# Optimization experiments

Measured on AMD Instinct MI355X. Metric: run time of the kernel, lower is better.

## Reference

```python
import jax, jax.numpy as jnp
import numpy as np

ORDER = 3  # polynomial filter order


def _sketch_conv(x, A, W, b, coeffs):
    # z = A @ (x W + b); out = sum_d coeffs[d-1] * z**d  (Horner-free power accumulation)
    z = A @ (x @ W + b)            # [N, out_c]
    p = z
    acc = coeffs[0] * z
    for d in range(1, ORDER):      # small fixed loop over polynomial order
        p = p * z
        acc = acc + coeffs[d] * p
    return acc


def setup_inputs() -> dict:
    key = jax.random.key(0)
    ks = jax.random.split(key, 12)
    N, C_IN, C_H, C_OUT = 8192, 128, 64, 40
    nf_mats = jax.random.normal(ks[0], (N, C_IN), dtype=jnp.float32)
    # scale by 1/sqrt(N) so polynomial powers stay O(1)
    conv_mats = jax.random.normal(ks[1], (N, N), dtype=jnp.float32) / np.float32(np.sqrt(N))
    def lin(k, fi, fo):
        kw, kb = jax.random.split(k)
        W = jax.random.normal(kw, (fi, fo), dtype=jnp.float32) / np.float32(np.sqrt(fi))
        b = jax.random.normal(kb, (fo,), dtype=jnp.float32) * np.float32(0.01)
        return W, b
    W1, b1 = lin(ks[2], C_IN, C_H)
    W2, b2 = lin(ks[3], C_H, C_H)
    W3, b3 = lin(ks[4], C_H, C_OUT)
    base = jnp.array([1.0, 0.0, 0.0], dtype=jnp.float32)
    c1 = base + jax.random.normal(ks[5], (ORDER,), dtype=jnp.float32) * 0.05
    c2 = base + jax.random.normal(ks[6], (ORDER,), dtype=jnp.float32) * 0.05
    c3 = base + jax.random.normal(ks[7], (ORDER,), dtype=jnp.float32) * 0.05
    return {"nf_mats": nf_mats, "conv_mats": conv_mats,
            "W1": W1, "b1": b1, "c1": c1,
            "W2": W2, "b2": b2, "c2": c2,
            "W3": W3, "b3": b3, "c3": c3}


def reference(nf_mats, conv_mats, W1, b1, c1, W2, b2, c2, W3, b3, c3):
    # SketchGCN eval-mode forward: batchnorm=False, dropout inactive.
    x = _sketch_conv(nf_mats, conv_mats, W1, b1, c1)      # first layer
    x = x + _sketch_conv(x, conv_mats, W2, b2, c2)        # residual middle layer
    return _sketch_conv(x, conv_mats, W3, b3, c3)         # output layer
```

## Files before the change

kernel.cpp:

```cpp
#include <hip/hip_runtime.h>
#include <stdint.h>

typedef __bf16 bf16x8 __attribute__((ext_vector_type(8)));
typedef float f32x4 __attribute__((ext_vector_type(4)));

using gvoid = const __attribute__((address_space(1))) void;
using lvoid = __attribute__((address_space(3))) void;

__device__ __forceinline__ unsigned short f2bf(float f) {
    union { float f; unsigned u; } x; x.f = f;
    unsigned u = x.u;
    u += 0x7FFFu + ((u >> 16) & 1u);
    return (unsigned short)(u >> 16);
}

__global__ void convert_bf16(const float* __restrict__ in,
                             unsigned short* __restrict__ out, int nv4) {
    int idx = blockIdx.x * blockDim.x + threadIdx.x;
    int stride = gridDim.x * blockDim.x;
    const float4* in4 = (const float4*)in;
    ushort4* out4 = (ushort4*)out;
    for (int i = idx; i < nv4; i += stride) {
        float4 v = in4[i];
        ushort4 o;
        o.x = f2bf(v.x); o.y = f2bf(v.y); o.z = f2bf(v.z); o.w = f2bf(v.w);
        out4[i] = o;
    }
}

template <int CIN>
__global__ __launch_bounds__(256) void small_gemm(const float* __restrict__ X,
                                                  const float* __restrict__ W,
                                                  const float* __restrict__ b,
                                                  int cout,
                                                  unsigned short* __restrict__ Yt) {
    __shared__ float Xs[64 * (CIN + 1)];
    __shared__ float Ws[CIN * 64];
    __shared__ float bs[64];
    const int t = threadIdx.x;
    const int i0 = blockIdx.x * 64;

    for (int e = t; e < 64 * CIN; e += 256) {
        int r = e / CIN, c = e % CIN;
        Xs[r * (CIN + 1) + c] = X[(size_t)(i0 + r) * CIN + c];
    }
    for (int e = t; e < CIN * 64; e += 256) {
        int k = e >> 6, j = e & 63;
        Ws[e] = (j < cout) ? W[k * cout + j] : 0.0f;
    }
    if (t < 64) bs[t] = (t < cout) ? b[t] : 0.0f;
    __syncthreads();

    const int i = t & 63;
    const int jg = t >> 6;
    float acc[16];
#pragma unroll
    for (int jj = 0; jj < 16; ++jj) acc[jj] = 0.0f;

    for (int k = 0; k < CIN; ++k) {
        float xv = Xs[i * (CIN + 1) + k];
        const float4* wr = (const float4*)&Ws[k * 64 + jg * 16];
#pragma unroll
        for (int q = 0; q < 4; ++q) {
            float4 w = wr[q];
            acc[q * 4 + 0] += xv * w.x;
            acc[q * 4 + 1] += xv * w.y;
            acc[q * 4 + 2] += xv * w.z;
            acc[q * 4 + 3] += xv * w.w;
        }
    }
#pragma unroll
    for (int jj = 0; jj < 16; ++jj) {
        int j = jg * 16 + jj;
        Yt[(size_t)j * 8192 + i0 + i] = f2bf(acc[jj] + bs[j]);
    }
}

__global__ __launch_bounds__(256) void big_gemm(const unsigned short* __restrict__ Ab,
                                                const unsigned short* __restrict__ Yt,
                                                float* __restrict__ P) {
    __shared__ unsigned short As[2][128 * 64];
    __shared__ unsigned short Bs[2][64 * 64];
    const int t = threadIdx.x;
    const int lane = t & 63, wid = t >> 6;
    const int lane15 = lane & 15, lane4 = lane >> 4;
    const int wm = wid >> 1, wn = wid & 1;
    const int row0 = blockIdx.x * 128;
    const int kbase = blockIdx.y * 2048;

    f32x4 acc[4][2];
    const f32x4 z4 = {0.f, 0.f, 0.f, 0.f};
#pragma unroll
    for (int m = 0; m < 4; ++m)
#pragma unroll
        for (int n = 0; n < 2; ++n) acc[m][n] = z4;

    auto stage = [&](int nb, int kt) {
#pragma unroll
        for (int ii = 0; ii < 4; ++ii) {
            int p = ii * 256 + wid * 64 + lane;
            int r = p >> 3;
            int c = (p & 7) ^ (r & 7);
            const unsigned short* gp = Ab + (size_t)(row0 + r) * 8192 + (kt + c * 8);
            unsigned short* lp = &As[nb][(ii * 256 + wid * 64) * 8];
            __builtin_amdgcn_global_load_lds((gvoid*)gp, (lvoid*)lp, 16, 0, 0);
        }
#pragma unroll
        for (int ii = 0; ii < 2; ++ii) {
            int q = ii * 256 + wid * 64 + lane;
            int n = q >> 3;
            int c = (q & 7) ^ (n & 7);
            const unsigned short* gp = Yt + (size_t)n * 8192 + (kt + c * 8);
            unsigned short* lp = &Bs[nb][(ii * 256 + wid * 64) * 8];
            __builtin_amdgcn_global_load_lds((gvoid*)gp, (lvoid*)lp, 16, 0, 0);
        }
    };

    stage(0, kbase);
    __syncthreads();
    int buf = 0;
    for (int tt = 0; tt < 32; ++tt) {
        if (tt + 1 < 32) stage(buf ^ 1, kbase + (tt + 1) * 64);
#pragma unroll
        for (int ks = 0; ks < 2; ++ks) {
            bf16x8 af[4], bfr[2];
#pragma unroll
            for (int m = 0; m < 4; ++m) {
                int r = wm * 64 + m * 16 + lane15;
                int c = ks * 4 + lane4;
                af[m] = *(const bf16x8*)&As[buf][((r << 3) | (c ^ (r & 7))) << 3];
            }
#pragma unroll
            for (int n = 0; n < 2; ++n) {
                int rn = wn * 32 + n * 16 + lane15;
                int c = ks * 4 + lane4;
                bfr[n] = *(const bf16x8*)&Bs[buf][((rn << 3) | (c ^ (rn & 7))) << 3];
            }
#pragma unroll
            for (int m = 0; m < 4; ++m)
#pragma unroll
                for (int n = 0; n < 2; ++n)
                    acc[m][n] = __builtin_amdgcn_mfma_f32_16x16x32_bf16(
                        af[m], bfr[n], acc[m][n], 0, 0, 0);
        }
        __syncthreads();
        buf ^= 1;
    }

    float* Po = P + (size_t)blockIdx.y * (8192 * 64);
#pragma unroll
    for (int m = 0; m < 4; ++m) {
        int r = row0 + wm * 64 + m * 16 + lane4 * 4;
#pragma unroll
        for (int n = 0; n < 2; ++n) {
            int cc = wn * 32 + n * 16 + lane15;
#pragma unroll
            for (int q = 0; q < 4; ++q)
                Po[(size_t)(r + q) * 64 + cc] = acc[m][n][q];
        }
    }
}

template <int MODE>
__global__ void reduce_poly(const float* __restrict__ P, const float* __restrict__ cf,
                            const float* __restrict__ xres, float* __restrict__ out) {
    int t = blockIdx.x * 256 + threadIdx.x;
    const int NT = 8192 * 64;
    float z = P[t] + P[t + NT] + P[t + 2 * NT] + P[t + 3 * NT];
    float c0 = cf[0], c1 = cf[1], c2 = cf[2];
    float v = z * (c0 + z * (c1 + z * c2));
    if (MODE == 1) v += xres[t];
    if (MODE == 2) {
        int i = t >> 6, j = t & 63;
        if (j < 40) out[(size_t)i * 40 + j] = v;
    } else {
        out[t] = v;
    }
}

extern "C" void kernel_launch(void* const* d_in, const int* in_sizes, int n_in,
                              void* d_out, int out_size, void* d_ws, size_t ws_size,
                              hipStream_t stream) {
    const float* nf   = (const float*)d_in[0];
    const float* Amat = (const float*)d_in[1];
    const float* W1   = (const float*)d_in[2];
    const float* b1   = (const float*)d_in[3];
    const float* c1   = (const float*)d_in[4];
    const float* W2   = (const float*)d_in[5];
    const float* b2   = (const float*)d_in[6];
    const float* c2   = (const float*)d_in[7];
    const float* W3   = (const float*)d_in[8];
    const float* b3   = (const float*)d_in[9];
    const float* c3   = (const float*)d_in[10];
    float* out = (float*)d_out;

    char* ws = (char*)d_ws;
    unsigned short* Abf = (unsigned short*)(ws);
    unsigned short* Yt  = (unsigned short*)(ws + 134217728);
    float* X1           = (float*)(ws + 135266304);
    float* X2           = (float*)(ws + 137363456);
    float* Pp           = (float*)(ws + 139460608);

    convert_bf16<<<4096, 256, 0, stream>>>(Amat, Abf, 8192 * 8192 / 4);

    small_gemm<128><<<128, 256, 0, stream>>>(nf, W1, b1, 64, Yt);
    big_gemm<<<dim3(64, 4), 256, 0, stream>>>(Abf, Yt, Pp);
    reduce_poly<0><<<2048, 256, 0, stream>>>(Pp, c1, nullptr, X1);

    small_gemm<64><<<128, 256, 0, stream>>>(X1, W2, b2, 64, Yt);
    big_gemm<<<dim3(64, 4), 256, 0, stream>>>(Abf, Yt, Pp);
    reduce_poly<1><<<2048, 256, 0, stream>>>(Pp, c2, X1, X2);

    small_gemm<64><<<128, 256, 0, stream>>>(X2, W3, b3, 40, Yt);
    big_gemm<<<dim3(64, 4), 256, 0, stream>>>(Abf, Yt, Pp);
    reduce_poly<2><<<2048, 256, 0, stream>>>(Pp, c3, nullptr, out);
}
```

Before: 247.9 us.

## Fuse bf16 conversion into first GEMM, fuse reduce with next small GEMM, widen split-K

The first big GEMM now reads the fp32 adjacency matrix directly, converts it to bf16 in registers, writes it to LDS and also stores the bf16 copy to global memory for the later layers. This drops the separate conversion pass over the 256MB matrix. The polynomial reduction is fused with the following small GEMM, removing a kernel and a round trip through X2. Split-K goes from 4 to 8 (grid 64x8), which doubles the partial-sum traffic in exchange for more parallelism. The residual is updated in place in X1.

```diff
diff --git a/kernel.cpp b/kernel.cpp
--- a/kernel.cpp
+++ b/kernel.cpp
@@ -13,19 +13,8 @@
     u += 0x7FFFu + ((u >> 16) & 1u);
     return (unsigned short)(u >> 16);
 }
-
-__global__ void convert_bf16(const float* __restrict__ in,
-                             unsigned short* __restrict__ out, int nv4) {
-    int idx = blockIdx.x * blockDim.x + threadIdx.x;
-    int stride = gridDim.x * blockDim.x;
-    const float4* in4 = (const float4*)in;
-    ushort4* out4 = (ushort4*)out;
-    for (int i = idx; i < nv4; i += stride) {
-        float4 v = in4[i];
-        ushort4 o;
-        o.x = f2bf(v.x); o.y = f2bf(v.y); o.z = f2bf(v.z); o.w = f2bf(v.w);
-        out4[i] = o;
-    }
+__device__ __forceinline__ unsigned pack2(float lo, float hi) {
+    return ((unsigned)f2bf(hi) << 16) | (unsigned)f2bf(lo);
 }
 
 template <int CIN>
@@ -76,7 +65,9 @@
     }
 }
 
-__global__ __launch_bounds__(256) void big_gemm(const unsigned short* __restrict__ Ab,
+template <int CONV>
+__global__ __launch_bounds__(256) void big_gemm(const float* __restrict__ Afp,
+                                                unsigned short* __restrict__ Ab,
                                                 const unsigned short* __restrict__ Yt,
                                                 float* __restrict__ P) {
     __shared__ unsigned short As[2][128 * 64];
@@ -86,7 +77,7 @@
     const int lane15 = lane & 15, lane4 = lane >> 4;
     const int wm = wid >> 1, wn = wid & 1;
     const int row0 = blockIdx.x * 128;
-    const int kbase = blockIdx.y * 2048;
+    const int kbase = blockIdx.y * 1024;
 
     f32x4 acc[4][2];
     const f32x4 z4 = {0.f, 0.f, 0.f, 0.f};
@@ -95,7 +86,33 @@
 #pragma unroll
         for (int n = 0; n < 2; ++n) acc[m][n] = z4;
 
-    auto stage = [&](int nb, int kt) {
+    float4 ra[4][2];
+
+    auto loadA_regs = [&](int kt) {
+#pragma unroll
+        for (int ii = 0; ii < 4; ++ii) {
+            int p = ii * 256 + t;
+            int r = p >> 3, cl = p & 7;
+            const float* gp = Afp + (size_t)(row0 + r) * 8192 + kt + cl * 8;
+            ra[ii][0] = *(const float4*)gp;
+            ra[ii][1] = *(const float4*)(gp + 4);
+        }
+    };
+    auto writeA = [&](int nb, int kt) {
+#pragma unroll
+        for (int ii = 0; ii < 4; ++ii) {
+            int p = ii * 256 + t;
+            int r = p >> 3, cl = p & 7;
+            uint4 ch;
+            ch.x = pack2(ra[ii][0].x, ra[ii][0].y);
+            ch.y = pack2(ra[ii][0].z, ra[ii][0].w);
+            ch.z = pack2(ra[ii][1].x, ra[ii][1].y);
+            ch.w = pack2(ra[ii][1].z, ra[ii][1].w);
+            *(uint4*)&As[nb][((r << 3) | (cl ^ (r & 7))) << 3] = ch;
+            *(uint4*)&Ab[(size_t)(row0 + r) * 8192 + kt + cl * 8] = ch;
+        }
+    };
+    auto stageA = [&](int nb, int kt) {
 #pragma unroll
         for (int ii = 0; ii < 4; ++ii) {
             int p = ii * 256 + wid * 64 + lane;
@@ -105,6 +122,8 @@
             unsigned short* lp = &As[nb][(ii * 256 + wid * 64) * 8];
             __builtin_amdgcn_global_load_lds((gvoid*)gp, (lvoid*)lp, 16, 0, 0);
         }
+    };
+    auto stageB = [&](int nb, int kt) {
 #pragma unroll
         for (int ii = 0; ii < 2; ++ii) {
             int q = ii * 256 + wid * 64 + lane;
@@ -116,11 +135,30 @@
         }
     };
 
-    stage(0, kbase);
+    if (CONV) {
+        loadA_regs(kbase);
+        stageB(0, kbase);
+        writeA(0, kbase);
+    } else {
+        stageA(0, kbase);
+        stageB(0, kbase);
+    }
     __syncthreads();
+
     int buf = 0;
-    for (int tt = 0; tt < 32; ++tt) {
-        if (tt + 1 < 32) stage(buf ^ 1, kbase + (tt + 1) * 64);
+    const int NIT = 16;
+    for (int tt = 0; tt < NIT; ++tt) {
+        const bool pre = (tt + 1 < NIT);
+        const int kt1 = kbase + (tt + 1) * 64;
+        if (pre) {
+            if (CONV) {
+                loadA_regs(kt1);
+                stageB(buf ^ 1, kt1);
+            } else {
+                stageA(buf ^ 1, kt1);
+                stageB(buf ^ 1, kt1);
+            }
+        }
 #pragma unroll
         for (int ks = 0; ks < 2; ++ks) {
             bf16x8 af[4], bfr[2];
@@ -143,6 +181,7 @@
                     acc[m][n] = __builtin_amdgcn_mfma_f32_16x16x32_bf16(
                         af[m], bfr[n], acc[m][n], 0, 0, 0);
         }
+        if (CONV && pre) writeA(buf ^ 1, kt1);
         __syncthreads();
         buf ^= 1;
     }
@@ -162,20 +201,76 @@
 }
 
 template <int MODE>
-__global__ void reduce_poly(const float* __restrict__ P, const float* __restrict__ cf,
-                            const float* __restrict__ xres, float* __restrict__ out) {
+__global__ __launch_bounds__(256) void fused_reduce(const float* __restrict__ P,
+                                                    const float* __restrict__ cf,
+                                                    const float* __restrict__ Wn,
+                                                    const float* __restrict__ bn,
+                                                    int cout,
+                                                    float* __restrict__ X1,
+                                                    unsigned short* __restrict__ Yt) {
+    __shared__ float Xs[64 * 65];
+    __shared__ float Ws[64 * 64];
+    __shared__ float bs[64];
+    const int t = threadIdx.x;
+    const int i0 = blockIdx.x * 64;
+    const size_t NT = 8192 * 64;
+
+    for (int e = t; e < 64 * 64; e += 256) {
+        int k = e >> 6, j = e & 63;
+        Ws[e] = (j < cout) ? Wn[k * cout + j] : 0.0f;
+    }
+    if (t < 64) bs[t] = (t < cout) ? bn[t] : 0.0f;
+    const float c0 = cf[0], c1 = cf[1], c2 = cf[2];
+
+    for (int s = 0; s < 16; ++s) {
+        int e = s * 256 + t;
+        int i = e >> 6, j = e & 63;
+        size_t base = (size_t)(i0 + i) * 64 + j;
+        float z = 0.f;
+#pragma unroll
+        for (int ks = 0; ks < 8; ++ks) z += P[ks * NT + base];
+        float v = z * (c0 + z * (c1 + z * c2));
+        if (MODE == 0) X1[base] = v;
+        else           v += X1[base];
+        Xs[i * 65 + j] = v;
+    }
+    __syncthreads();
+
+    const int i = t & 63;
+    const int jg = t >> 6;
+    float acc[16];
+#pragma unroll
+    for (int jj = 0; jj < 16; ++jj) acc[jj] = 0.0f;
+    for (int k = 0; k < 64; ++k) {
+        float xv = Xs[i * 65 + k];
+        const float4* wr = (const float4*)&Ws[k * 64 + jg * 16];
+#pragma unroll
+        for (int q = 0; q < 4; ++q) {
+            float4 w = wr[q];
+            acc[q * 4 + 0] += xv * w.x;
+            acc[q * 4 + 1] += xv * w.y;
+            acc[q * 4 + 2] += xv * w.z;
+            acc[q * 4 + 3] += xv * w.w;
+        }
+    }
+#pragma unroll
+    for (int jj = 0; jj < 16; ++jj) {
+        int j = jg * 16 + jj;
+        Yt[(size_t)j * 8192 + i0 + i] = f2bf(acc[jj] + bs[j]);
+    }
+}
+
+__global__ void reduce_out(const float* __restrict__ P, const float* __restrict__ cf,
+                           float* __restrict__ out) {
     int t = blockIdx.x * 256 + threadIdx.x;
-    const int NT = 8192 * 64;
-    float z = P[t] + P[t + NT] + P[t + 2 * NT] + P[t + 3 * NT];
+    const size_t NT = 8192 * 64;
+    float z = 0.f;
+#pragma unroll
+    for (int ks = 0; ks < 8; ++ks) z += P[ks * NT + t];
     float c0 = cf[0], c1 = cf[1], c2 = cf[2];
     float v = z * (c0 + z * (c1 + z * c2));
-    if (MODE == 1) v += xres[t];
-    if (MODE == 2) {
-        int i = t >> 6, j = t & 63;
-        if (j < 40) out[(size_t)i * 40 + j] = v;
-    } else {
-        out[t] = v;
-    }
+    int i = t >> 6, j = t & 63;
+    if (j < 40) out[(size_t)i * 40 + j] = v;
 }
 
 extern "C" void kernel_launch(void* const* d_in, const int* in_sizes, int n_in,
@@ -198,20 +293,15 @@
     unsigned short* Abf = (unsigned short*)(ws);
     unsigned short* Yt  = (unsigned short*)(ws + 134217728);
     float* X1           = (float*)(ws + 135266304);
-    float* X2           = (float*)(ws + 137363456);
-    float* Pp           = (float*)(ws + 139460608);
-
-    convert_bf16<<<4096, 256, 0, stream>>>(Amat, Abf, 8192 * 8192 / 4);
+    float* Pp           = (float*)(ws + 137363456);
 
     small_gemm<128><<<128, 256, 0, stream>>>(nf, W1, b1, 64, Yt);
-    big_gemm<<<dim3(64, 4), 256, 0, stream>>>(Abf, Yt, Pp);
-    reduce_poly<0><<<2048, 256, 0, stream>>>(Pp, c1, nullptr, X1);
-
-    small_gemm<64><<<128, 256, 0, stream>>>(X1, W2, b2, 64, Yt);
-    big_gemm<<<dim3(64, 4), 256, 0, stream>>>(Abf, Yt, Pp);
-    reduce_poly<1><<<2048, 256, 0, stream>>>(Pp, c2, X1, X2);
-
-    small_gemm<64><<<128, 256, 0, stream>>>(X2, W3, b3, 40, Yt);
-    big_gemm<<<dim3(64, 4), 256, 0, stream>>>(Abf, Yt, Pp);
-    reduce_poly<2><<<2048, 256, 0, stream>>>(Pp, c3, nullptr, out);
-}
+    big_gemm<1><<<dim3(64, 8), 256, 0, stream>>>(Amat, Abf, Yt, Pp);
+    fused_reduce<0><<<128, 256, 0, stream>>>(Pp, c1, W2, b2, 64, X1, Yt);
+
+    big_gemm<0><<<dim3(64, 8), 256, 0, stream>>>(nullptr, Abf, Yt, Pp);
+    fused_reduce<1><<<128, 256, 0, stream>>>(Pp, c2, W3, b3, 40, X1, Yt);
+
+    big_gemm<0><<<dim3(64, 8), 256, 0, stream>>>(nullptr, Abf, Yt, Pp);
+    reduce_out<<<2048, 256, 0, stream>>>(Pp, c3, out);
+}
```

Result: faster. 212.9 us (-14.1%).
